# Kernel tuning notes

Measured on AMD Instinct MI355X. Metric: run time of the kernel, lower is better.

The kernel has to match this reference:

```python
import jax, jax.numpy as jnp
import numpy as np


def setup_inputs() -> dict:
    key = jax.random.key(0)
    k1, k2, k3 = jax.random.split(key, 3)
    B, H, W, Cin, Cout = 8, 256, 256, 8, 8
    Fh, Fw = 2 * H - 1, 2 * W - 1  # SAME padding, unit strides -> kernel size 2k-1
    inputs = jax.random.normal(k1, (B, H, W, Cin), dtype=jnp.float32)
    # Kernel is parameterized directly in Fourier space; leading axis 2 = (real, imag).
    kernel = jax.random.normal(k2, (2, Fh, Fw, Cin, Cout), dtype=jnp.float32) * 0.01
    bias = jax.random.normal(k3, (Cout,), dtype=jnp.float32) * 0.01
    return {"inputs": inputs, "kernel": kernel, "bias": bias}


def reference(inputs, kernel, bias):
    # inputs: (B, H, W, Cin); kernel: (2, 2H-1, 2W-1, Cin, Cout); bias: (Cout,)
    B, H, W, Cin = inputs.shape
    Fh, Fw = 2 * H - 1, 2 * W - 1
    complex_kernel = jax.lax.complex(kernel[0], kernel[1])  # (Fh, Fw, Cin, Cout)
    # Zero-pad spatial dims to (2H-1, 2W-1) and FFT (s= pads at the end, same as jnp.pad).
    xf = jnp.fft.fftn(inputs, s=(Fh, Fw), axes=(1, 2))  # (B, Fh, Fw, Cin) complex
    # Contract over in_features in frequency space (linearity of IFFT makes this
    # mathematically identical to ifft-then-sum of the original, but avoids the
    # huge (B, Fh, Fw, Cin, Cout) intermediate).
    yf = jnp.einsum("bhwi,hwio->bhwo", xf, complex_kernel)
    y = jnp.fft.ifftn(yf, axes=(1, 2)).real  # (B, Fh, Fw, Cout)
    # SAME crop: centered slice of size (H, W).
    sh = (Fh - H) // 2
    sw = (Fw - W) // 2
    y = y[:, sh:sh + H, sw:sw + W, :]
    return y + bias
```

## Files before the change

kernel.cpp:

```cpp
#include <hip/hip_runtime.h>

#define TPB 256


typedef _Float16 half8  __attribute__((ext_vector_type(8)));
typedef _Float16 half2v __attribute__((ext_vector_type(2)));
typedef float    floatx16 __attribute__((ext_vector_type(16)));
typedef unsigned int uintx4 __attribute__((ext_vector_type(4)));

__device__ __forceinline__ void split16(float v, _Float16& h, _Float16& l) {
    h = (_Float16)v;
    l = (_Float16)(v - (float)h);
}

__global__ __launch_bounds__(TPB)
void build_tables_k(_Float16* __restrict__ At, _Float16* __restrict__ Ct,
                    _Float16* __restrict__ C2) {
    int idx = blockIdx.x * TPB + threadIdx.x;
    const float w = (float)(6.28318530717958647692 / 511.0);
    {
        int k = idx >> 8, n = idx & 255;
        float cr = 0.f, ci = 0.f;
        if (k < 511) {
            int m = (k * n) % 511;
            float s, c; sincosf(w * (float)m, &s, &c);
            cr = c; ci = -s;
        }
        _Float16 h, l;
        split16(cr, h, l); At[idx] = h; At[131072 + idx] = l;
        split16(ci, h, l); At[262144 + idx] = h; At[393216 + idx] = l;
    }
    {
        int p = idx >> 9, k1 = idx & 511;
        float cr = 0.f, ci = 0.f;
        if (k1 < 511) {
            int m = (k1 * (p + 127)) % 511;
            float s, c; sincosf(w * (float)m, &s, &c);
            cr = c; ci = s;
        }
        _Float16 h, l;
        split16(cr, h, l); Ct[idx] = h; Ct[131072 + idx] = l;
        split16(ci, h, l); Ct[262144 + idx] = h; Ct[393216 + idx] = l;
    }
    if (idx < 65536) {
        int q = idx >> 8, k2 = idx & 255;
        int m = (k2 * (q + 127)) % 511;
        float s, c; sincosf(w * (float)m, &s, &c);
        _Float16 h, l;
        split16(c, h, l); C2[idx] = h; C2[65536 + idx] = l;
        split16(s, h, l); C2[131072 + idx] = h; C2[196608 + idx] = l;
    }
}

__global__ __launch_bounds__(TPB)
void txp_k(const float* __restrict__ x, _Float16* __restrict__ xT) {
    __shared__ _Float16 L[8][2][32][34];
    const int tid = threadIdx.x;
    const int b = blockIdx.z, n0 = blockIdx.y * 32, w0 = blockIdx.x * 32;
    #pragma unroll
    for (int pp = 0; pp < 4; pp++) {
        int w = tid & 31, n = pp * 8 + (tid >> 5);
        const float4* src = (const float4*)(x + ((size_t)((b * 256 + n0 + n) * 256) + w0 + w) * 8);
        float4 v0 = src[0], v1 = src[1];
        float vv[8] = {v0.x, v0.y, v0.z, v0.w, v1.x, v1.y, v1.z, v1.w};
        #pragma unroll
        for (int ch = 0; ch < 8; ch++) {
            _Float16 h, lo; split16(vv[ch], h, lo);
            L[ch][0][w][n] = h;
            L[ch][1][w][n] = lo;
        }
    }
    __syncthreads();
    #pragma unroll
    for (int rr = 0; rr < 2; rr++) {
        int r = tid * 2 + rr;
        int ch = r >> 6, pl = (r >> 5) & 1, w = r & 31;
        const _Float16* row = &L[ch][pl][w][0];
        size_t off = ((size_t)((b * 8 + ch) * 2 + pl)) * 65536 + (size_t)(w0 + w) * 256 + n0;
        #pragma unroll
        for (int cc = 0; cc < 4; cc++) {
            uintx4 u;
            #pragma unroll
            for (int c = 0; c < 4; c++) u[c] = *(const unsigned int*)(row + cc * 8 + c * 2);
            *(uintx4*)(xT + off + cc * 8) = u;
        }
    }
}

__global__ __launch_bounds__(TPB)
void ksym_k(const float* __restrict__ Kr, const float* __restrict__ Ki,
            float* __restrict__ KeR, float* __restrict__ KeI) {
    __shared__ float LR[64][65];
    __shared__ float LI[64][65];
    const int tid = threadIdx.x;
    const int k2  = blockIdx.x >> 3;
    const int k1g = (blockIdx.x & 7) * 64;
    const int k2m = (k2 == 0) ? 0 : 511 - k2;
    const float sc = (k2 == 0) ? 0.5f : 1.0f;
    #pragma unroll
    for (int t = 0; t < 4; t++) {
        int idx = tid + t * 256;
        int j = idx & 15, k1l = idx >> 4;
        int k1 = k1g + k1l;
        float4 rs = {0,0,0,0}, rm = {0,0,0,0}, is = {0,0,0,0}, im = {0,0,0,0};
        if (k1 < 511) {
            int k1m = (k1 == 0) ? 0 : 511 - k1;
            size_t so = ((size_t)(k1  * 511 + k2 )) * 64 + j * 4;
            size_t mo = ((size_t)(k1m * 511 + k2m)) * 64 + j * 4;
            rs = *(const float4*)(Kr + so);
            rm = *(const float4*)(Kr + mo);
            is = *(const float4*)(Ki + so);
            im = *(const float4*)(Ki + mo);
        }
        LR[j*4+0][k1l] = sc * (rs.x + rm.x);
        LR[j*4+1][k1l] = sc * (rs.y + rm.y);
        LR[j*4+2][k1l] = sc * (rs.z + rm.z);
        LR[j*4+3][k1l] = sc * (rs.w + rm.w);
        LI[j*4+0][k1l] = sc * (is.x - im.x);
        LI[j*4+1][k1l] = sc * (is.y - im.y);
        LI[j*4+2][k1l] = sc * (is.z - im.z);
        LI[j*4+3][k1l] = sc * (is.w - im.w);
    }
    __syncthreads();
    const size_t ob = (size_t)k2 * 512 + k1g;
    #pragma unroll
    for (int t = 0; t < 4; t++) {
        int idx = tid + t * 256;
        int io = idx >> 4, fq = idx & 15;
        float4 vr = make_float4(LR[io][fq*4], LR[io][fq*4+1], LR[io][fq*4+2], LR[io][fq*4+3]);
        float4 vi = make_float4(LI[io][fq*4], LI[io][fq*4+1], LI[io][fq*4+2], LI[io][fq*4+3]);
        *(float4*)(KeR + (size_t)io * 131072 + ob + fq * 4) = vr;
        *(float4*)(KeI + (size_t)io * 131072 + ob + fq * 4) = vi;
    }
}

template<bool BREAL, bool DREAL>
__global__ __launch_bounds__(TPB, 2)
void mgemm_k(int K,
             const _Float16* __restrict__ Ap, long sAz, long sAp,
             const _Float16* __restrict__ Bp, long sBz, long sBp,
             _Float16* __restrict__ Dp, long sDz, long sDp, int Dn,
             float* __restrict__ Df, long sFz)
{
    __shared__ _Float16 sm[24576];

    const int tid = threadIdx.x;
    const int bm = blockIdx.y * 128, bn = blockIdx.x * 128;
    const int z = blockIdx.z;
    const _Float16* A = Ap + (size_t)z * sAz;
    const _Float16* B = Bp + (size_t)z * sBz;

    const int l  = tid & 63;
    const int wv = tid >> 6;
    const int lr = l & 31, lg = l >> 5;
    const int wm = (wv >> 1) * 64, wn = (wv & 1) * 64;

    floatx16 accR[2][2], accI[2][2];
    #pragma unroll
    for (int i = 0; i < 2; i++)
        #pragma unroll
        for (int j = 0; j < 2; j++)
            #pragma unroll
            for (int r = 0; r < 16; r++) {
                accR[i][j][r] = 0.f;
                accI[i][j][r] = 0.f;
            }

    const _Float16* aPtr[4];
    int aLds[4];
    #pragma unroll
    for (int j = 0; j < 4; j++) {
        int c = tid + j * 256;
        int p = c >> 8, rem = c & 255, row = rem >> 1, kq = rem & 1;
        aPtr[j] = A + (size_t)p * sAp + (size_t)(bm + row) * K + kq * 8;
        aLds[j] = p * 3072 + row * 24 + ((kq ^ (((row >> 3) ^ (row >> 4)) & 1)) * 8);
    }
    const int NBC = BREAL ? 2 : 4;
    const _Float16* bPtr[4];
    int bLds[4];
    #pragma unroll
    for (int j = 0; j < 4; j++) {
        if (j < NBC) {
            int c = tid + j * 256;
            int p = c >> 8, rem = c & 255, col = rem >> 1, kq = rem & 1;
            bPtr[j] = B + (size_t)p * sBp + (size_t)(bn + col) * K + kq * 8;
            bLds[j] = 12288 + p * 3072 + col * 24 + ((kq ^ (((col >> 3) ^ (col >> 4)) & 1)) * 8);
        }
    }

    int aOff[2][4], bOff[2][4];
    #pragma unroll
    for (int mt = 0; mt < 2; mt++) {
        int R = wm + mt * 32 + lr;
        int sw = ((R >> 3) ^ (R >> 4)) & 1;
        #pragma unroll
        for (int p = 0; p < 4; p++)
            aOff[mt][p] = p * 3072 + R * 24 + ((lg ^ sw) * 8);
    }
    #pragma unroll
    for (int nt = 0; nt < 2; nt++) {
        int Cc = wn + nt * 32 + lr;
        int sw = ((Cc >> 3) ^ (Cc >> 4)) & 1;
        #pragma unroll
        for (int p = 0; p < 4; p++)
            bOff[nt][p] = 12288 + p * 3072 + Cc * 24 + ((lg ^ sw) * 8);
    }

    for (int k0 = 0; k0 < K; k0 += 16) {
        #pragma unroll
        for (int j = 0; j < 4; j++) {
            uintx4 v = *(const uintx4*)aPtr[j]; aPtr[j] += 16;
            *(uintx4*)(sm + aLds[j]) = v;
        }
        #pragma unroll
        for (int j = 0; j < 4; j++) {
            if (j < NBC) {
                uintx4 v = *(const uintx4*)bPtr[j]; bPtr[j] += 16;
                *(uintx4*)(sm + bLds[j]) = v;
            }
        }
        __syncthreads();

        half8 a[2][4];
        #pragma unroll
        for (int mt = 0; mt < 2; mt++)
            #pragma unroll
            for (int p = 0; p < 4; p++)
                a[mt][p] = *(const half8*)(sm + aOff[mt][p]);

        half8 nai[2][2];
        if constexpr (!BREAL) {
            #pragma unroll
            for (int mt = 0; mt < 2; mt++)
                #pragma unroll
                for (int p = 0; p < 2; p++) {
                    uintx4 u = __builtin_bit_cast(uintx4, a[mt][2 + p]);
                    u ^= 0x80008000u;
                    nai[mt][p] = __builtin_bit_cast(half8, u);
                }
        }

        #pragma unroll
        for (int nt = 0; nt < 2; nt++) {
            half8 b0 = *(const half8*)(sm + bOff[nt][0]);
            half8 b1 = *(const half8*)(sm + bOff[nt][1]);
            half8 b2, b3;
            if constexpr (!BREAL) {
                b2 = *(const half8*)(sm + bOff[nt][2]);
                b3 = *(const half8*)(sm + bOff[nt][3]);
            }
            #pragma unroll
            for (int mt = 0; mt < 2; mt++) {
                if constexpr (BREAL) {
                    accR[mt][nt] = __builtin_amdgcn_mfma_f32_32x32x16_f16(a[mt][0], b0, accR[mt][nt], 0, 0, 0);
                    accR[mt][nt] = __builtin_amdgcn_mfma_f32_32x32x16_f16(a[mt][0], b1, accR[mt][nt], 0, 0, 0);
                    accR[mt][nt] = __builtin_amdgcn_mfma_f32_32x32x16_f16(a[mt][1], b0, accR[mt][nt], 0, 0, 0);
                    accI[mt][nt] = __builtin_amdgcn_mfma_f32_32x32x16_f16(a[mt][2], b0, accI[mt][nt], 0, 0, 0);
                    accI[mt][nt] = __builtin_amdgcn_mfma_f32_32x32x16_f16(a[mt][2], b1, accI[mt][nt], 0, 0, 0);
                    accI[mt][nt] = __builtin_amdgcn_mfma_f32_32x32x16_f16(a[mt][3], b0, accI[mt][nt], 0, 0, 0);
                } else if constexpr (DREAL) {
                    accR[mt][nt] = __builtin_amdgcn_mfma_f32_32x32x16_f16(a[mt][0], b0, accR[mt][nt], 0, 0, 0);
                    accR[mt][nt] = __builtin_amdgcn_mfma_f32_32x32x16_f16(a[mt][0], b1, accR[mt][nt], 0, 0, 0);
                    accR[mt][nt] = __builtin_amdgcn_mfma_f32_32x32x16_f16(a[mt][1], b0, accR[mt][nt], 0, 0, 0);
                    accR[mt][nt] = __builtin_amdgcn_mfma_f32_32x32x16_f16(nai[mt][0], b2, accR[mt][nt], 0, 0, 0);
                    accR[mt][nt] = __builtin_amdgcn_mfma_f32_32x32x16_f16(nai[mt][0], b3, accR[mt][nt], 0, 0, 0);
                    accR[mt][nt] = __builtin_amdgcn_mfma_f32_32x32x16_f16(nai[mt][1], b2, accR[mt][nt], 0, 0, 0);
                } else {
                    accR[mt][nt] = __builtin_amdgcn_mfma_f32_32x32x16_f16(a[mt][0], b0, accR[mt][nt], 0, 0, 0);
                    accR[mt][nt] = __builtin_amdgcn_mfma_f32_32x32x16_f16(a[mt][0], b1, accR[mt][nt], 0, 0, 0);
                    accR[mt][nt] = __builtin_amdgcn_mfma_f32_32x32x16_f16(a[mt][1], b0, accR[mt][nt], 0, 0, 0);
                    accR[mt][nt] = __builtin_amdgcn_mfma_f32_32x32x16_f16(nai[mt][0], b2, accR[mt][nt], 0, 0, 0);
                    accR[mt][nt] = __builtin_amdgcn_mfma_f32_32x32x16_f16(nai[mt][0], b3, accR[mt][nt], 0, 0, 0);
                    accR[mt][nt] = __builtin_amdgcn_mfma_f32_32x32x16_f16(nai[mt][1], b2, accR[mt][nt], 0, 0, 0);
                    accI[mt][nt] = __builtin_amdgcn_mfma_f32_32x32x16_f16(a[mt][0], b2, accI[mt][nt], 0, 0, 0);
                    accI[mt][nt] = __builtin_amdgcn_mfma_f32_32x32x16_f16(a[mt][0], b3, accI[mt][nt], 0, 0, 0);
                    accI[mt][nt] = __builtin_amdgcn_mfma_f32_32x32x16_f16(a[mt][1], b2, accI[mt][nt], 0, 0, 0);
                    accI[mt][nt] = __builtin_amdgcn_mfma_f32_32x32x16_f16(a[mt][2], b0, accI[mt][nt], 0, 0, 0);
                    accI[mt][nt] = __builtin_amdgcn_mfma_f32_32x32x16_f16(a[mt][2], b1, accI[mt][nt], 0, 0, 0);
                    accI[mt][nt] = __builtin_amdgcn_mfma_f32_32x32x16_f16(a[mt][3], b0, accI[mt][nt], 0, 0, 0);
                }
            }
        }
        __syncthreads();
    }

    if constexpr (DREAL) {
        float* D = Df + (size_t)z * sFz;
        #pragma unroll
        for (int mt = 0; mt < 2; mt++)
            #pragma unroll
            for (int nt = 0; nt < 2; nt++)
                #pragma unroll
                for (int r = 0; r < 16; r++) {
                    int row = bm + wm + mt * 32 + (r & 3) + 8 * (r >> 2) + 4 * lg;
                    int col = bn + wn + nt * 32 + lr;
                    D[(size_t)row * Dn + col] = accR[mt][nt][r];
                }
    } else {
        _Float16* D = Dp + (size_t)z * sDz;
        #pragma unroll
        for (int mt = 0; mt < 2; mt++)
            #pragma unroll
            for (int nt = 0; nt < 2; nt++)
                #pragma unroll
                for (int r = 0; r < 16; r++) {
                    int row = bm + wm + mt * 32 + (r & 3) + 8 * (r >> 2) + 4 * lg;
                    int col = bn + wn + nt * 32 + lr;
                    size_t base = (size_t)row * Dn + col;
                    _Float16 h, lo;
                    split16(accR[mt][nt][r], h, lo);
                    D[base] = h;
                    D[sDp + base] = lo;
                    split16(accI[mt][nt][r], h, lo);
                    D[2 * sDp + base] = h;
                    D[3 * sDp + base] = lo;
                }
    }
}

__global__ __launch_bounds__(TPB)
void einsum_k(_Float16* __restrict__ F, const float* __restrict__ KeR,
              const float* __restrict__ KeI, int g)
{
    const int pt = (blockIdx.x * TPB + threadIdx.x) * 2;
    for (int b = 0; b < g; b++) {
        _Float16* Fb = F + (size_t)b * 4194304;
        float xr0[8], xr1[8], xi0[8], xi1[8];
        #pragma unroll
        for (int i = 0; i < 8; i++) {
            const _Float16* P = Fb + (size_t)i * 524288 + pt;
            half2v rh = *(const half2v*)(P);
            half2v rl = *(const half2v*)(P + 131072);
            half2v ih = *(const half2v*)(P + 262144);
            half2v il = *(const half2v*)(P + 393216);
            xr0[i] = (float)rh.x + (float)rl.x;
            xr1[i] = (float)rh.y + (float)rl.y;
            xi0[i] = (float)ih.x + (float)il.x;
            xi1[i] = (float)ih.y + (float)il.y;
        }
        #pragma unroll
        for (int o = 0; o < 8; o++) {
            float ar0 = 0.f, ar1 = 0.f, ai0 = 0.f, ai1 = 0.f;
            #pragma unroll
            for (int i = 0; i < 8; i++) {
                const size_t ko = (size_t)(i * 8 + o) * 131072 + pt;
                float2 kr = *(const float2*)(KeR + ko);
                float2 ki = *(const float2*)(KeI + ko);
                ar0 = fmaf(xr0[i], kr.x, ar0); ar0 = fmaf(-xi0[i], ki.x, ar0);
                ai0 = fmaf(xr0[i], ki.x, ai0); ai0 = fmaf(xi0[i], kr.x, ai0);
                ar1 = fmaf(xr1[i], kr.y, ar1); ar1 = fmaf(-xi1[i], ki.y, ar1);
                ai1 = fmaf(xr1[i], ki.y, ai1); ai1 = fmaf(xi1[i], kr.y, ai1);
            }
            _Float16* Q = Fb + (size_t)o * 524288 + pt;
            _Float16 h0, l0, h1, l1;
            split16(ar0, h0, l0); split16(ar1, h1, l1);
            { half2v v = {h0, h1}; *(half2v*)(Q) = v; }
            { half2v v = {l0, l1}; *(half2v*)(Q + 131072) = v; }
            split16(ai0, h0, l0); split16(ai1, h1, l1);
            { half2v v = {h0, h1}; *(half2v*)(Q + 262144) = v; }
            { half2v v = {l0, l1}; *(half2v*)(Q + 393216) = v; }
        }
    }
}

__global__ __launch_bounds__(TPB)
void tout_k(const float* __restrict__ Dq, const float* __restrict__ bias,
            float* __restrict__ out, int b0)
{
    int idx = blockIdx.x * TPB + threadIdx.x;
    int o = idx & 7, q = (idx >> 3) & 255, p = (idx >> 11) & 255, bl = idx >> 19;
    float v = Dq[(size_t)(bl * 8 + o) * 65536 + p * 256 + q];
    out[(size_t)(b0 + bl) * 524288 + (size_t)(idx & 524287)] = v * (1.f / 261121.f) + bias[o];
}


extern "C" void kernel_launch(void* const* d_in, const int* in_sizes, int n_in,
                              void* d_out, int out_size, void* d_ws, size_t ws_size,
                              hipStream_t stream) {
    const float* x    = (const float*)d_in[0];
    const float* Kr   = (const float*)d_in[1];
    const float* Ki   = Kr + 16711744;
    const float* bias = (const float*)d_in[2];
    float* out = (float*)d_out;
    char* ws = (char*)d_ws;

    _Float16* Atab = (_Float16*)(ws + 0);
    _Float16* Ctab = (_Float16*)(ws + 1048576);
    _Float16* Ct2  = (_Float16*)(ws + 2097152);
    _Float16* xTp  = (_Float16*)(ws + 2621440);
    float*    KeR  = (float*)   (ws + 19398656);
    float*    KeI  = (float*)   (ws + 52953088);
    const size_t fixedEnd = 86507520;

    int g = 1;
    for (int cand = 8; cand >= 1; cand >>= 1) {
        if (fixedEnd + (size_t)cand * 16777216 <= ws_size) { g = cand; break; }
    }
    _Float16* F1  = (_Float16*)(ws + fixedEnd);
    _Float16* F2T = (_Float16*)(ws + fixedEnd + (size_t)g * 8388608);
    _Float16* F1b = F1;
    float*    Dq  = (float*)F2T;

    build_tables_k<<<512, TPB, 0, stream>>>(Atab, Ctab, Ct2);
    txp_k<<<dim3(8, 8, 8), TPB, 0, stream>>>(x, xTp);
    ksym_k<<<2048, TPB, 0, stream>>>(Kr, Ki, KeR, KeI);

    for (int b0 = 0; b0 < 8; b0 += g) {
        int Z = g * 8;
        mgemm_k<true, false><<<dim3(2, 4, Z), TPB, 0, stream>>>(
            256, Atab, 0, 131072,
            xTp + (size_t)b0 * 8 * 131072, 131072, 65536,
            F1, 524288, 131072, 256, nullptr, 0);

        mgemm_k<false, false><<<dim3(4, 2, Z), TPB, 0, stream>>>(
            256, Atab, 0, 131072,
            F1, 524288, 131072,
            F2T, 524288, 131072, 512, nullptr, 0);

        einsum_k<<<256, TPB, 0, stream>>>(F2T, KeR, KeI, g);

        mgemm_k<false, false><<<dim3(2, 2, Z), TPB, 0, stream>>>(
            512, Ctab, 0, 131072,
            F2T, 524288, 131072,
            F1b, 262144, 65536, 256, nullptr, 0);

        mgemm_k<false, true><<<dim3(2, 2, Z), TPB, 0, stream>>>(
            256, F1b, 262144, 65536,
            Ct2, 0, 65536,
            nullptr, 0, 0, 256, Dq, 65536);

        tout_k<<<g * 2048, TPB, 0, stream>>>(Dq, bias, out, b0);
    }
}
```

Measured before the change: 509.5 us.

## Pre-swizzle DFT tables into MFMA fragment layout and interleave data planes

Stores the twiddle tables in per-lane MFMA fragment order so the GEMM kernel reads them straight from global memory into registers, without staging them in LDS. The data operand is stored with its hi/lo/real/imag planes interleaved per 8-element chunk, so each load pulls contiguous 16-byte vectors. A register prefetch of the next K-tile is added, and the einsum kernel is reworked to batch four images per kernel load. This cuts LDS traffic and the shared-memory footprint, but twiddle fetches now depend on L2/L1 hits and every producer and consumer indexing has to match the new layout.

```diff
diff --git a/kernel.cpp b/kernel.cpp
--- a/kernel.cpp
+++ b/kernel.cpp
@@ -4,7 +4,6 @@
 
 
 typedef _Float16 half8  __attribute__((ext_vector_type(8)));
-typedef _Float16 half2v __attribute__((ext_vector_type(2)));
 typedef float    floatx16 __attribute__((ext_vector_type(16)));
 typedef unsigned int uintx4 __attribute__((ext_vector_type(4)));
 
@@ -18,43 +17,44 @@
                     _Float16* __restrict__ C2) {
     int idx = blockIdx.x * TPB + threadIdx.x;
     const float w = (float)(6.28318530717958647692 / 511.0);
-    {
-        int k = idx >> 8, n = idx & 255;
+    _Float16* T; int R, kc2, K; int mode;
+    if (idx < 16384)      { T = At; R = idx >> 5;  kc2 = idx & 31; K = 256; mode = 0; }
+    else if (idx < 32768) { int id = idx - 16384; T = Ct; R = id >> 6; kc2 = id & 63; K = 512; mode = 1; }
+    else                  { int id = idx - 32768; T = C2; R = id >> 5; kc2 = id & 31; K = 256; mode = 2; }
+
+    half8 vrh, vrl, vih, vil;
+    #pragma unroll
+    for (int j = 0; j < 8; j++) {
+        int k = kc2 * 8 + j;
         float cr = 0.f, ci = 0.f;
-        if (k < 511) {
-            int m = (k * n) % 511;
-            float s, c; sincosf(w * (float)m, &s, &c);
-            cr = c; ci = -s;
-        }
-        _Float16 h, l;
-        split16(cr, h, l); At[idx] = h; At[131072 + idx] = l;
-        split16(ci, h, l); At[262144 + idx] = h; At[393216 + idx] = l;
-    }
-    {
-        int p = idx >> 9, k1 = idx & 511;
-        float cr = 0.f, ci = 0.f;
-        if (k1 < 511) {
-            int m = (k1 * (p + 127)) % 511;
-            float s, c; sincosf(w * (float)m, &s, &c);
-            cr = c; ci = s;
-        }
-        _Float16 h, l;
-        split16(cr, h, l); Ct[idx] = h; Ct[131072 + idx] = l;
-        split16(ci, h, l); Ct[262144 + idx] = h; Ct[393216 + idx] = l;
-    }
-    if (idx < 65536) {
-        int q = idx >> 8, k2 = idx & 255;
-        int m = (k2 * (q + 127)) % 511;
-        float s, c; sincosf(w * (float)m, &s, &c);
-        _Float16 h, l;
-        split16(c, h, l); C2[idx] = h; C2[65536 + idx] = l;
-        split16(s, h, l); C2[131072 + idx] = h; C2[196608 + idx] = l;
-    }
+        if (mode == 0) {
+            if (R < 511) {
+                int m = (R * k) % 511;
+                float s, c; sincosf(w * (float)m, &s, &c);
+                cr = c; ci = -s;
+            }
+        } else {
+            if (!(mode == 1 && k == 511)) {
+                int m = (k * (R + 127)) % 511;
+                float s, c; sincosf(w * (float)m, &s, &c);
+                cr = c; ci = s;
+            }
+        }
+        _Float16 th, tl;
+        split16(cr, th, tl); vrh[j] = th; vrl[j] = tl;
+        split16(ci, th, tl); vih[j] = th; vil[j] = tl;
+    }
+    int tile = R >> 5, kcblk = kc2 >> 1, lane = (R & 31) + 32 * (kc2 & 1);
+    size_t base = ((size_t)(tile * (K >> 4) + kcblk) * 4) * 512 + lane * 8;
+    *(half8*)(T + base)        = vrh;
+    *(half8*)(T + base + 512)  = vrl;
+    *(half8*)(T + base + 1024) = vih;
+    *(half8*)(T + base + 1536) = vil;
 }
 
 __global__ __launch_bounds__(TPB)
 void txp_k(const float* __restrict__ x, _Float16* __restrict__ xT) {
-    __shared__ _Float16 L[8][2][32][34];
+    __shared__ _Float16 L[8][2][32][40];
     const int tid = threadIdx.x;
     const int b = blockIdx.z, n0 = blockIdx.y * 32, w0 = blockIdx.x * 32;
     #pragma unroll
@@ -72,18 +72,13 @@
     }
     __syncthreads();
     #pragma unroll
-    for (int rr = 0; rr < 2; rr++) {
-        int r = tid * 2 + rr;
-        int ch = r >> 6, pl = (r >> 5) & 1, w = r & 31;
-        const _Float16* row = &L[ch][pl][w][0];
-        size_t off = ((size_t)((b * 8 + ch) * 2 + pl)) * 65536 + (size_t)(w0 + w) * 256 + n0;
-        #pragma unroll
-        for (int cc = 0; cc < 4; cc++) {
-            uintx4 u;
-            #pragma unroll
-            for (int c = 0; c < 4; c++) u[c] = *(const unsigned int*)(row + cc * 8 + c * 2);
-            *(uintx4*)(xT + off + cc * 8) = u;
-        }
+    for (int t = 0; t < 8; t++) {
+        int c = tid + t * 256;
+        int p = c & 1, cc = (c >> 1) & 3, w = (c >> 3) & 31, ch = c >> 8;
+        uintx4 v = *(const uintx4*)&L[ch][p][w][cc * 8];
+        size_t off = ((size_t)(b * 8 + ch)) * 131072 + (size_t)(w0 + w) * 512
+                   + (size_t)((n0 >> 3) + cc) * 16 + p * 8;
+        *(uintx4*)(xT + off) = v;
     }
 }
 
@@ -134,26 +129,57 @@
     }
 }
 
-template<bool BREAL, bool DREAL>
+template<int NPD, bool TBA, bool DREAL>
 __global__ __launch_bounds__(TPB, 2)
-void mgemm_k(int K,
-             const _Float16* __restrict__ Ap, long sAz, long sAp,
-             const _Float16* __restrict__ Bp, long sBz, long sBp,
-             _Float16* __restrict__ Dp, long sDz, long sDp, int Dn,
-             float* __restrict__ Df, long sFz)
+void mgemm_k(int K, const _Float16* __restrict__ Tf,
+             const _Float16* __restrict__ Dd, long sDz,
+             _Float16* __restrict__ Out, long sOz, int OutKc,
+             float* __restrict__ Of, long sOfz, int OfN)
 {
-    __shared__ _Float16 sm[24576];
+    constexpr int SLOTS = NPD * 2;
+    constexpr int CPT   = NPD;
+    __shared__ _Float16 sm[128 * SLOTS * 8];
 
     const int tid = threadIdx.x;
     const int bm = blockIdx.y * 128, bn = blockIdx.x * 128;
     const int z = blockIdx.z;
-    const _Float16* A = Ap + (size_t)z * sAz;
-    const _Float16* B = Bp + (size_t)z * sBz;
+    const _Float16* D = Dd + (size_t)z * sDz;
 
     const int l  = tid & 63;
     const int wv = tid >> 6;
     const int lr = l & 31, lg = l >> 5;
     const int wm = (wv >> 1) * 64, wn = (wv & 1) * 64;
+    const int Kc16 = K >> 4;
+
+    const int tb = (TBA ? bm + wm : bn + wn);
+    int tTB[2];
+    #pragma unroll
+    for (int t = 0; t < 2; t++) tTB[t] = ((tb + t * 32) >> 5) * Kc16;
+
+    const int db = (TBA ? wn : wm);
+    int dOff[2][NPD];
+    #pragma unroll
+    for (int t = 0; t < 2; t++) {
+        int cl = db + t * 32 + lr;
+        int sw = cl & (SLOTS - 1);
+        #pragma unroll
+        for (int p = 0; p < NPD; p++)
+            dOff[t][p] = cl * (NPD * 16) + (((p * 2 + lg) ^ sw) * 8);
+    }
+
+    const int bSide = (TBA ? bn : bm);
+    const _Float16* gP[CPT];
+    int lO[CPT];
+    #pragma unroll
+    for (int j = 0; j < CPT; j++) {
+        int cid = tid + j * TPB;
+        int col = cid / SLOTS;
+        int inner = cid & (SLOTS - 1);
+        int p = inner & (NPD - 1);
+        int h = inner / NPD;
+        gP[j] = D + ((size_t)(bSide + col) * (K >> 3) + h) * (NPD * 8) + p * 8;
+        lO[j] = col * (NPD * 16) + (((p * 2 + h) ^ (col & (SLOTS - 1))) * 8);
+    }
 
     floatx16 accR[2][2], accI[2][2];
     #pragma unroll
@@ -161,131 +187,101 @@
         #pragma unroll
         for (int j = 0; j < 2; j++)
             #pragma unroll
-            for (int r = 0; r < 16; r++) {
-                accR[i][j][r] = 0.f;
-                accI[i][j][r] = 0.f;
-            }
-
-    const _Float16* aPtr[4];
-    int aLds[4];
-    #pragma unroll
-    for (int j = 0; j < 4; j++) {
-        int c = tid + j * 256;
-        int p = c >> 8, rem = c & 255, row = rem >> 1, kq = rem & 1;
-        aPtr[j] = A + (size_t)p * sAp + (size_t)(bm + row) * K + kq * 8;
-        aLds[j] = p * 3072 + row * 24 + ((kq ^ (((row >> 3) ^ (row >> 4)) & 1)) * 8);
-    }
-    const int NBC = BREAL ? 2 : 4;
-    const _Float16* bPtr[4];
-    int bLds[4];
-    #pragma unroll
-    for (int j = 0; j < 4; j++) {
-        if (j < NBC) {
-            int c = tid + j * 256;
-            int p = c >> 8, rem = c & 255, col = rem >> 1, kq = rem & 1;
-            bPtr[j] = B + (size_t)p * sBp + (size_t)(bn + col) * K + kq * 8;
-            bLds[j] = 12288 + p * 3072 + col * 24 + ((kq ^ (((col >> 3) ^ (col >> 4)) & 1)) * 8);
-        }
-    }
-
-    int aOff[2][4], bOff[2][4];
-    #pragma unroll
-    for (int mt = 0; mt < 2; mt++) {
-        int R = wm + mt * 32 + lr;
-        int sw = ((R >> 3) ^ (R >> 4)) & 1;
-        #pragma unroll
-        for (int p = 0; p < 4; p++)
-            aOff[mt][p] = p * 3072 + R * 24 + ((lg ^ sw) * 8);
-    }
-    #pragma unroll
-    for (int nt = 0; nt < 2; nt++) {
-        int Cc = wn + nt * 32 + lr;
-        int sw = ((Cc >> 3) ^ (Cc >> 4)) & 1;
-        #pragma unroll
-        for (int p = 0; p < 4; p++)
-            bOff[nt][p] = 12288 + p * 3072 + Cc * 24 + ((lg ^ sw) * 8);
-    }
+            for (int r = 0; r < 16; r++) { accR[i][j][r] = 0.f; accI[i][j][r] = 0.f; }
+
+    uintx4 st[CPT];
+    #pragma unroll
+    for (int j = 0; j < CPT; j++) { st[j] = *(const uintx4*)gP[j]; gP[j] += NPD * 16; }
 
     for (int k0 = 0; k0 < K; k0 += 16) {
         #pragma unroll
-        for (int j = 0; j < 4; j++) {
-            uintx4 v = *(const uintx4*)aPtr[j]; aPtr[j] += 16;
-            *(uintx4*)(sm + aLds[j]) = v;
-        }
-        #pragma unroll
-        for (int j = 0; j < 4; j++) {
-            if (j < NBC) {
-                uintx4 v = *(const uintx4*)bPtr[j]; bPtr[j] += 16;
-                *(uintx4*)(sm + bLds[j]) = v;
-            }
-        }
+        for (int j = 0; j < CPT; j++) *(uintx4*)(sm + lO[j]) = st[j];
         __syncthreads();
-
-        half8 a[2][4];
-        #pragma unroll
-        for (int mt = 0; mt < 2; mt++)
+        if (k0 + 16 < K) {
+            #pragma unroll
+            for (int j = 0; j < CPT; j++) { st[j] = *(const uintx4*)gP[j]; gP[j] += NPD * 16; }
+        }
+
+        const int kc0 = k0 >> 4;
+        half8 tf[2][4];
+        #pragma unroll
+        for (int t = 0; t < 2; t++)
             #pragma unroll
             for (int p = 0; p < 4; p++)
-                a[mt][p] = *(const half8*)(sm + aOff[mt][p]);
-
-        half8 nai[2][2];
-        if constexpr (!BREAL) {
-            #pragma unroll
-            for (int mt = 0; mt < 2; mt++)
+                tf[t][p] = *(const half8*)(Tf + ((size_t)(tTB[t] + kc0) * 4 + p) * 512 + l * 8);
+        half8 df[2][NPD];
+        #pragma unroll
+        for (int t = 0; t < 2; t++)
+            #pragma unroll
+            for (int p = 0; p < NPD; p++)
+                df[t][p] = *(const half8*)(sm + dOff[t][p]);
+
+        if constexpr (TBA && NPD == 4 && !DREAL) {
+            half8 na[2][2];
+            #pragma unroll
+            for (int t = 0; t < 2; t++)
                 #pragma unroll
                 for (int p = 0; p < 2; p++) {
-                    uintx4 u = __builtin_bit_cast(uintx4, a[mt][2 + p]);
+                    uintx4 u = __builtin_bit_cast(uintx4, tf[t][2 + p]);
                     u ^= 0x80008000u;
-                    nai[mt][p] = __builtin_bit_cast(half8, u);
-                }
-        }
-
-        #pragma unroll
-        for (int nt = 0; nt < 2; nt++) {
-            half8 b0 = *(const half8*)(sm + bOff[nt][0]);
-            half8 b1 = *(const half8*)(sm + bOff[nt][1]);
-            half8 b2, b3;
-            if constexpr (!BREAL) {
-                b2 = *(const half8*)(sm + bOff[nt][2]);
-                b3 = *(const half8*)(sm + bOff[nt][3]);
-            }
-            #pragma unroll
-            for (int mt = 0; mt < 2; mt++) {
-                if constexpr (BREAL) {
-                    accR[mt][nt] = __builtin_amdgcn_mfma_f32_32x32x16_f16(a[mt][0], b0, accR[mt][nt], 0, 0, 0);
-                    accR[mt][nt] = __builtin_amdgcn_mfma_f32_32x32x16_f16(a[mt][0], b1, accR[mt][nt], 0, 0, 0);
-                    accR[mt][nt] = __builtin_amdgcn_mfma_f32_32x32x16_f16(a[mt][1], b0, accR[mt][nt], 0, 0, 0);
-                    accI[mt][nt] = __builtin_amdgcn_mfma_f32_32x32x16_f16(a[mt][2], b0, accI[mt][nt], 0, 0, 0);
-                    accI[mt][nt] = __builtin_amdgcn_mfma_f32_32x32x16_f16(a[mt][2], b1, accI[mt][nt], 0, 0, 0);
-                    accI[mt][nt] = __builtin_amdgcn_mfma_f32_32x32x16_f16(a[mt][3], b0, accI[mt][nt], 0, 0, 0);
-                } else if constexpr (DREAL) {
-                    accR[mt][nt] = __builtin_amdgcn_mfma_f32_32x32x16_f16(a[mt][0], b0, accR[mt][nt], 0, 0, 0);
-                    accR[mt][nt] = __builtin_amdgcn_mfma_f32_32x32x16_f16(a[mt][0], b1, accR[mt][nt], 0, 0, 0);
-                    accR[mt][nt] = __builtin_amdgcn_mfma_f32_32x32x16_f16(a[mt][1], b0, accR[mt][nt], 0, 0, 0);
-                    accR[mt][nt] = __builtin_amdgcn_mfma_f32_32x32x16_f16(nai[mt][0], b2, accR[mt][nt], 0, 0, 0);
-                    accR[mt][nt] = __builtin_amdgcn_mfma_f32_32x32x16_f16(nai[mt][0], b3, accR[mt][nt], 0, 0, 0);
-                    accR[mt][nt] = __builtin_amdgcn_mfma_f32_32x32x16_f16(nai[mt][1], b2, accR[mt][nt], 0, 0, 0);
-                } else {
-                    accR[mt][nt] = __builtin_amdgcn_mfma_f32_32x32x16_f16(a[mt][0], b0, accR[mt][nt], 0, 0, 0);
-                    accR[mt][nt] = __builtin_amdgcn_mfma_f32_32x32x16_f16(a[mt][0], b1, accR[mt][nt], 0, 0, 0);
-                    accR[mt][nt] = __builtin_amdgcn_mfma_f32_32x32x16_f16(a[mt][1], b0, accR[mt][nt], 0, 0, 0);
-                    accR[mt][nt] = __builtin_amdgcn_mfma_f32_32x32x16_f16(nai[mt][0], b2, accR[mt][nt], 0, 0, 0);
-                    accR[mt][nt] = __builtin_amdgcn_mfma_f32_32x32x16_f16(nai[mt][0], b3, accR[mt][nt], 0, 0, 0);
-                    accR[mt][nt] = __builtin_amdgcn_mfma_f32_32x32x16_f16(nai[mt][1], b2, accR[mt][nt], 0, 0, 0);
-                    accI[mt][nt] = __builtin_amdgcn_mfma_f32_32x32x16_f16(a[mt][0], b2, accI[mt][nt], 0, 0, 0);
-                    accI[mt][nt] = __builtin_amdgcn_mfma_f32_32x32x16_f16(a[mt][0], b3, accI[mt][nt], 0, 0, 0);
-                    accI[mt][nt] = __builtin_amdgcn_mfma_f32_32x32x16_f16(a[mt][1], b2, accI[mt][nt], 0, 0, 0);
-                    accI[mt][nt] = __builtin_amdgcn_mfma_f32_32x32x16_f16(a[mt][2], b0, accI[mt][nt], 0, 0, 0);
-                    accI[mt][nt] = __builtin_amdgcn_mfma_f32_32x32x16_f16(a[mt][2], b1, accI[mt][nt], 0, 0, 0);
-                    accI[mt][nt] = __builtin_amdgcn_mfma_f32_32x32x16_f16(a[mt][3], b0, accI[mt][nt], 0, 0, 0);
-                }
-            }
+                    na[t][p] = __builtin_bit_cast(half8, u);
+                }
+            #pragma unroll
+            for (int nt = 0; nt < 2; nt++)
+                #pragma unroll
+                for (int mt = 0; mt < 2; mt++) {
+                    accR[mt][nt] = __builtin_amdgcn_mfma_f32_32x32x16_f16(tf[mt][0], df[nt][0], accR[mt][nt], 0,0,0);
+                    accR[mt][nt] = __builtin_amdgcn_mfma_f32_32x32x16_f16(tf[mt][0], df[nt][1], accR[mt][nt], 0,0,0);
+                    accR[mt][nt] = __builtin_amdgcn_mfma_f32_32x32x16_f16(tf[mt][1], df[nt][0], accR[mt][nt], 0,0,0);
+                    accR[mt][nt] = __builtin_amdgcn_mfma_f32_32x32x16_f16(na[mt][0], df[nt][2], accR[mt][nt], 0,0,0);
+                    accR[mt][nt] = __builtin_amdgcn_mfma_f32_32x32x16_f16(na[mt][0], df[nt][3], accR[mt][nt], 0,0,0);
+                    accR[mt][nt] = __builtin_amdgcn_mfma_f32_32x32x16_f16(na[mt][1], df[nt][2], accR[mt][nt], 0,0,0);
+                    accI[mt][nt] = __builtin_amdgcn_mfma_f32_32x32x16_f16(tf[mt][0], df[nt][2], accI[mt][nt], 0,0,0);
+                    accI[mt][nt] = __builtin_amdgcn_mfma_f32_32x32x16_f16(tf[mt][0], df[nt][3], accI[mt][nt], 0,0,0);
+                    accI[mt][nt] = __builtin_amdgcn_mfma_f32_32x32x16_f16(tf[mt][1], df[nt][2], accI[mt][nt], 0,0,0);
+                    accI[mt][nt] = __builtin_amdgcn_mfma_f32_32x32x16_f16(tf[mt][2], df[nt][0], accI[mt][nt], 0,0,0);
+                    accI[mt][nt] = __builtin_amdgcn_mfma_f32_32x32x16_f16(tf[mt][2], df[nt][1], accI[mt][nt], 0,0,0);
+                    accI[mt][nt] = __builtin_amdgcn_mfma_f32_32x32x16_f16(tf[mt][3], df[nt][0], accI[mt][nt], 0,0,0);
+                }
+        } else if constexpr (TBA && NPD == 2) {
+            #pragma unroll
+            for (int nt = 0; nt < 2; nt++)
+                #pragma unroll
+                for (int mt = 0; mt < 2; mt++) {
+                    accR[mt][nt] = __builtin_amdgcn_mfma_f32_32x32x16_f16(tf[mt][0], df[nt][0], accR[mt][nt], 0,0,0);
+                    accR[mt][nt] = __builtin_amdgcn_mfma_f32_32x32x16_f16(tf[mt][0], df[nt][1], accR[mt][nt], 0,0,0);
+                    accR[mt][nt] = __builtin_amdgcn_mfma_f32_32x32x16_f16(tf[mt][1], df[nt][0], accR[mt][nt], 0,0,0);
+                    accI[mt][nt] = __builtin_amdgcn_mfma_f32_32x32x16_f16(tf[mt][2], df[nt][0], accI[mt][nt], 0,0,0);
+                    accI[mt][nt] = __builtin_amdgcn_mfma_f32_32x32x16_f16(tf[mt][2], df[nt][1], accI[mt][nt], 0,0,0);
+                    accI[mt][nt] = __builtin_amdgcn_mfma_f32_32x32x16_f16(tf[mt][3], df[nt][0], accI[mt][nt], 0,0,0);
+                }
+        } else {
+            half8 na[2][2];
+            #pragma unroll
+            for (int t = 0; t < 2; t++)
+                #pragma unroll
+                for (int p = 0; p < 2; p++) {
+                    uintx4 u = __builtin_bit_cast(uintx4, df[t][2 + p]);
+                    u ^= 0x80008000u;
+                    na[t][p] = __builtin_bit_cast(half8, u);
+                }
+            #pragma unroll
+            for (int nt = 0; nt < 2; nt++)
+                #pragma unroll
+                for (int mt = 0; mt < 2; mt++) {
+                    accR[mt][nt] = __builtin_amdgcn_mfma_f32_32x32x16_f16(df[mt][0], tf[nt][0], accR[mt][nt], 0,0,0);
+                    accR[mt][nt] = __builtin_amdgcn_mfma_f32_32x32x16_f16(df[mt][0], tf[nt][1], accR[mt][nt], 0,0,0);
+                    accR[mt][nt] = __builtin_amdgcn_mfma_f32_32x32x16_f16(df[mt][1], tf[nt][0], accR[mt][nt], 0,0,0);
+                    accR[mt][nt] = __builtin_amdgcn_mfma_f32_32x32x16_f16(na[mt][0], tf[nt][2], accR[mt][nt], 0,0,0);
+                    accR[mt][nt] = __builtin_amdgcn_mfma_f32_32x32x16_f16(na[mt][0], tf[nt][3], accR[mt][nt], 0,0,0);
+                    accR[mt][nt] = __builtin_amdgcn_mfma_f32_32x32x16_f16(na[mt][1], tf[nt][2], accR[mt][nt], 0,0,0);
+                }
         }
         __syncthreads();
     }
 
     if constexpr (DREAL) {
-        float* D = Df + (size_t)z * sFz;
+        float* Dv = Of + (size_t)z * sOfz;
         #pragma unroll
         for (int mt = 0; mt < 2; mt++)
             #pragma unroll
@@ -294,10 +290,10 @@
                 for (int r = 0; r < 16; r++) {
                     int row = bm + wm + mt * 32 + (r & 3) + 8 * (r >> 2) + 4 * lg;
                     int col = bn + wn + nt * 32 + lr;
-                    D[(size_t)row * Dn + col] = accR[mt][nt][r];
+                    Dv[(size_t)row * OfN + col] = accR[mt][nt][r];
                 }
     } else {
-        _Float16* D = Dp + (size_t)z * sDz;
+        _Float16* O = Out + (size_t)z * sOz;
         #pragma unroll
         for (int mt = 0; mt < 2; mt++)
             #pragma unroll
@@ -306,14 +302,14 @@
                 for (int r = 0; r < 16; r++) {
                     int row = bm + wm + mt * 32 + (r & 3) + 8 * (r >> 2) + 4 * lg;
                     int col = bn + wn + nt * 32 + lr;
-                    size_t base = (size_t)row * Dn + col;
+                    size_t base = ((size_t)row * OutKc + (col >> 3)) * 32 + (col & 7);
                     _Float16 h, lo;
                     split16(accR[mt][nt][r], h, lo);
-                    D[base] = h;
-                    D[sDp + base] = lo;
+                    O[base]      = h;
+                    O[base + 8]  = lo;
                     split16(accI[mt][nt][r], h, lo);
-                    D[2 * sDp + base] = h;
-                    D[3 * sDp + base] = lo;
+                    O[base + 16] = h;
+                    O[base + 24] = lo;
                 }
     }
 }
@@ -322,43 +318,46 @@
 void einsum_k(_Float16* __restrict__ F, const float* __restrict__ KeR,
               const float* __restrict__ KeI, int g)
 {
-    const int pt = (blockIdx.x * TPB + threadIdx.x) * 2;
-    for (int b = 0; b < g; b++) {
-        _Float16* Fb = F + (size_t)b * 4194304;
-        float xr0[8], xr1[8], xi0[8], xi1[8];
-        #pragma unroll
-        for (int i = 0; i < 8; i++) {
-            const _Float16* P = Fb + (size_t)i * 524288 + pt;
-            half2v rh = *(const half2v*)(P);
-            half2v rl = *(const half2v*)(P + 131072);
-            half2v ih = *(const half2v*)(P + 262144);
-            half2v il = *(const half2v*)(P + 393216);
-            xr0[i] = (float)rh.x + (float)rl.x;
-            xr1[i] = (float)rh.y + (float)rl.y;
-            xi0[i] = (float)ih.x + (float)il.x;
-            xi1[i] = (float)ih.y + (float)il.y;
+    const int pt = blockIdx.x * TPB + threadIdx.x;
+    const int k2 = pt >> 9, k1 = pt & 511;
+    const size_t fo = ((size_t)(k2 * 64 + (k1 >> 3))) * 32 + (k1 & 7);
+
+    for (int b0 = 0; b0 < g; b0 += 4) {
+        const int bt = (g - b0 < 4) ? (g - b0) : 4;
+        float xr[4][8], xi[4][8];
+        #pragma unroll
+        for (int bb = 0; bb < 4; bb++) {
+            if (bb >= bt) break;
+            #pragma unroll
+            for (int i = 0; i < 8; i++) {
+                const _Float16* P = F + ((size_t)((b0 + bb) * 8 + i)) * 524288 + fo;
+                xr[bb][i] = (float)P[0]  + (float)P[8];
+                xi[bb][i] = (float)P[16] + (float)P[24];
+            }
         }
         #pragma unroll
         for (int o = 0; o < 8; o++) {
-            float ar0 = 0.f, ar1 = 0.f, ai0 = 0.f, ai1 = 0.f;
+            float ar[4] = {0.f,0.f,0.f,0.f}, ai[4] = {0.f,0.f,0.f,0.f};
             #pragma unroll
             for (int i = 0; i < 8; i++) {
-                const size_t ko = (size_t)(i * 8 + o) * 131072 + pt;
-                float2 kr = *(const float2*)(KeR + ko);
-                float2 ki = *(const float2*)(KeI + ko);
-                ar0 = fmaf(xr0[i], kr.x, ar0); ar0 = fmaf(-xi0[i], ki.x, ar0);
-                ai0 = fmaf(xr0[i], ki.x, ai0); ai0 = fmaf(xi0[i], kr.x, ai0);
-                ar1 = fmaf(xr1[i], kr.y, ar1); ar1 = fmaf(-xi1[i], ki.y, ar1);
-                ai1 = fmaf(xr1[i], ki.y, ai1); ai1 = fmaf(xi1[i], kr.y, ai1);
+                float kr = KeR[(size_t)(i * 8 + o) * 131072 + pt];
+                float ki = KeI[(size_t)(i * 8 + o) * 131072 + pt];
+                #pragma unroll
+                for (int bb = 0; bb < 4; bb++) {
+                    ar[bb] = fmaf(xr[bb][i], kr, ar[bb]);
+                    ar[bb] = fmaf(-xi[bb][i], ki, ar[bb]);
+                    ai[bb] = fmaf(xr[bb][i], ki, ai[bb]);
+                    ai[bb] = fmaf(xi[bb][i], kr, ai[bb]);
+                }
             }
-            _Float16* Q = Fb + (size_t)o * 524288 + pt;
-            _Float16 h0, l0, h1, l1;
-            split16(ar0, h0, l0); split16(ar1, h1, l1);
-            { half2v v = {h0, h1}; *(half2v*)(Q) = v; }
-            { half2v v = {l0, l1}; *(half2v*)(Q + 131072) = v; }
-            split16(ai0, h0, l0); split16(ai1, h1, l1);
-            { half2v v = {h0, h1}; *(half2v*)(Q + 262144) = v; }
-            { half2v v = {l0, l1}; *(half2v*)(Q + 393216) = v; }
+            #pragma unroll
+            for (int bb = 0; bb < 4; bb++) {
+                if (bb >= bt) break;
+                _Float16* Q = F + ((size_t)((b0 + bb) * 8 + o)) * 524288 + fo;
+                _Float16 h, lo;
+                split16(ar[bb], h, lo); Q[0]  = h; Q[8]  = lo;
+                split16(ai[bb], h, lo); Q[16] = h; Q[24] = lo;
+            }
         }
     }
 }
@@ -384,12 +383,12 @@
     float* out = (float*)d_out;
     char* ws = (char*)d_ws;
 
-    _Float16* Atab = (_Float16*)(ws + 0);
-    _Float16* Ctab = (_Float16*)(ws + 1048576);
-    _Float16* Ct2  = (_Float16*)(ws + 2097152);
-    _Float16* xTp  = (_Float16*)(ws + 2621440);
-    float*    KeR  = (float*)   (ws + 19398656);
-    float*    KeI  = (float*)   (ws + 52953088);
+    _Float16* AtabF = (_Float16*)(ws + 0);
+    _Float16* CtabF = (_Float16*)(ws + 1048576);
+    _Float16* Ct2F  = (_Float16*)(ws + 2097152);
+    _Float16* xTp   = (_Float16*)(ws + 2621440);
+    float*    KeR   = (float*)   (ws + 19398656);
+    float*    KeI   = (float*)   (ws + 52953088);
     const size_t fixedEnd = 86507520;
 
     int g = 1;
@@ -401,33 +400,33 @@
     _Float16* F1b = F1;
     float*    Dq  = (float*)F2T;
 
-    build_tables_k<<<512, TPB, 0, stream>>>(Atab, Ctab, Ct2);
+    build_tables_k<<<160, TPB, 0, stream>>>(AtabF, CtabF, Ct2F);
     txp_k<<<dim3(8, 8, 8), TPB, 0, stream>>>(x, xTp);
     ksym_k<<<2048, TPB, 0, stream>>>(Kr, Ki, KeR, KeI);
 
     for (int b0 = 0; b0 < 8; b0 += g) {
         int Z = g * 8;
-        mgemm_k<true, false><<<dim3(2, 4, Z), TPB, 0, stream>>>(
-            256, Atab, 0, 131072,
-            xTp + (size_t)b0 * 8 * 131072, 131072, 65536,
-            F1, 524288, 131072, 256, nullptr, 0);
-
-        mgemm_k<false, false><<<dim3(4, 2, Z), TPB, 0, stream>>>(
-            256, Atab, 0, 131072,
-            F1, 524288, 131072,
-            F2T, 524288, 131072, 512, nullptr, 0);
-
-        einsum_k<<<256, TPB, 0, stream>>>(F2T, KeR, KeI, g);
-
-        mgemm_k<false, false><<<dim3(2, 2, Z), TPB, 0, stream>>>(
-            512, Ctab, 0, 131072,
-            F2T, 524288, 131072,
-            F1b, 262144, 65536, 256, nullptr, 0);
-
-        mgemm_k<false, true><<<dim3(2, 2, Z), TPB, 0, stream>>>(
-            256, F1b, 262144, 65536,
-            Ct2, 0, 65536,
-            nullptr, 0, 0, 256, Dq, 65536);
+        mgemm_k<2, true, false><<<dim3(2, 4, Z), TPB, 0, stream>>>(
+            256, AtabF,
+            xTp + (size_t)b0 * 8 * 131072, 131072,
+            F1, 524288, 32, nullptr, 0, 0);
+
+        mgemm_k<4, true, false><<<dim3(4, 2, Z), TPB, 0, stream>>>(
+            256, AtabF,
+            F1, 524288,
+            F2T, 524288, 64, nullptr, 0, 0);
+
+        einsum_k<<<512, TPB, 0, stream>>>(F2T, KeR, KeI, g);
+
+        mgemm_k<4, true, false><<<dim3(2, 2, Z), TPB, 0, stream>>>(
+            512, CtabF,
+            F2T, 524288,
+            F1b, 262144, 32, nullptr, 0, 0);
+
+        mgemm_k<4, false, true><<<dim3(2, 2, Z), TPB, 0, stream>>>(
+            256, Ct2F,
+            F1b, 262144,
+            nullptr, 0, 0, Dq, 65536, 256);
 
         tout_k<<<g * 2048, TPB, 0, stream>>>(Dq, bias, out, b0);
     }
```

New measurement: 504.5 us. Within noise of the previous version (-1.0%).
